# Optimization experiments

Hardware: AMD Instinct MI355X
Metric: run time of the kernel (lower is better)

Reference implementation:

```python
import jax, jax.numpy as jnp
import numpy as np

B = 16; DEMO = 5; COND = 50; QOI = 50
L = DEMO * (COND + 2 * QOI)  # 750
D = 1024; H = 16; HD = D // H; NL = 6; DFF = 4096
IN_DIM = 5; OUT_DIM = 2; MAXPOS = max(COND, QOI)
NEG = -1e9


def _build_consts():
    # token types per demo segment: 0=cond, 1=qoi_kv, 2=qoi_k (query)
    types, demo, pos = [], [], []
    for d in range(DEMO):
        types += [0] * COND + [1] * QOI + [2] * QOI
        demo += [d] * (COND + 2 * QOI)
        pos += list(range(COND)) + list(range(QOI)) + list(range(QOI))
    t = np.array(types); g = np.array(demo); p = np.array(pos)
    ti, tj = t[:, None], t[None, :]
    gi, gj = g[:, None], g[None, :]
    eye = np.arange(L)[:, None] == np.arange(L)[None, :]
    prev = (gj < gi) & (tj < 2)                      # attend to cond/qoi_kv of earlier demos
    same = (gj == gi) & ((tj == 0) | ((ti == 1) & (tj == 1)) | ((ti == 2) & eye))
    mask = prev | same                               # True = allowed
    out_idx = np.where(t == 2)[0]                    # qoi_k positions -> outputs
    return mask, p, out_idx


def setup_inputs():
    key = jax.random.key(0)
    ks = jax.random.split(key, 10)
    mask, pos, out_idx = _build_consts()
    s = 0.02
    return {
        'sequence': jax.random.normal(ks[0], (B, L, IN_DIM), jnp.float32),
        'pre_W': jax.random.normal(ks[1], (IN_DIM, D), jnp.float32) * s,
        'pre_b': jnp.zeros((D,), jnp.float32),
        'pe_table': jax.random.normal(ks[2], (MAXPOS, D), jnp.float32) * s,
        'Wqkv': jax.random.normal(ks[3], (NL, D, 3 * D), jnp.float32) * s,
        'bqkv': jnp.zeros((NL, 3 * D), jnp.float32),
        'Wo': jax.random.normal(ks[4], (NL, D, D), jnp.float32) * s,
        'bo': jnp.zeros((NL, D), jnp.float32),
        'ln1_g': jnp.ones((NL, D), jnp.float32), 'ln1_b': jnp.zeros((NL, D), jnp.float32),
        'ln2_g': jnp.ones((NL, D), jnp.float32), 'ln2_b': jnp.zeros((NL, D), jnp.float32),
        'W1': jax.random.normal(ks[5], (NL, D, DFF), jnp.float32) * s,
        'b1': jnp.zeros((NL, DFF), jnp.float32),
        'W2': jax.random.normal(ks[6], (NL, DFF, D), jnp.float32) * s,
        'b2': jnp.zeros((NL, D), jnp.float32),
        'post_W': jax.random.normal(ks[7], (D, OUT_DIM), jnp.float32) * s,
        'post_b': jnp.zeros((OUT_DIM,), jnp.float32),
        'basic_mask': jnp.asarray(mask),
        'index_pos': jnp.asarray(pos, jnp.int32),
        'out_idx': jnp.asarray(out_idx, jnp.int32),
    }


def _ln(x, g, b):
    m = jnp.mean(x, axis=-1, keepdims=True)
    v = jnp.var(x, axis=-1, keepdims=True)
    return (x - m) * jax.lax.rsqrt(v + 1e-5) * g + b


def _encoder(x, bias, Wqkv, bqkv, Wo, bo, ln1_g, ln1_b, ln2_g, ln2_b, W1, b1, W2, b2):
    scale = 1.0 / np.sqrt(HD)
    for l in range(NL):
        qkv = x @ Wqkv[l] + bqkv[l]                          # [B,L,3D]
        q, k, v = jnp.split(qkv, 3, axis=-1)
        hd = lambda t: t.reshape(B, L, H, HD).transpose(0, 2, 1, 3)
        q, k, v = hd(q), hd(k), hd(v)
        sc = jnp.einsum('bhqd,bhkd->bhqk', q, k) * scale + bias
        a = jax.nn.softmax(sc, axis=-1)
        o = jnp.einsum('bhqk,bhkd->bhqd', a, v).transpose(0, 2, 1, 3).reshape(B, L, D)
        x = _ln(x + o @ Wo[l] + bo[l], ln1_g[l], ln1_b[l])   # post-LN (torch default)
        h = jax.nn.gelu(x @ W1[l] + b1[l], approximate=False)
        x = _ln(x + h @ W2[l] + b2[l], ln2_g[l], ln2_b[l])
    return x


def reference(sequence, pre_W, pre_b, pe_table, Wqkv, bqkv, Wo, bo,
              ln1_g, ln1_b, ln2_g, ln2_b, W1, b1, W2, b2,
              post_W, post_b, basic_mask, index_pos, out_idx):
    x = sequence @ pre_W + pre_b + pe_table[index_pos]       # pre-projection + learned PE
    bias = jnp.where(basic_mask, 0.0, NEG)[None, None, :, :]  # ~basic_mask -> -inf additive
    x = _encoder(x, bias, Wqkv, bqkv, Wo, bo, ln1_g, ln1_b, ln2_g, ln2_b, W1, b1, W2, b2)
    y = x @ post_W + post_b                                  # [B,L,OUT_DIM]
    y = y[:, out_idx, :]                                     # select qoi_k outputs
    return y.reshape(B, DEMO, QOI, OUT_DIM)
```

## Files before the change

kernel.cpp:

```cpp
#include <hip/hip_runtime.h>


#define Bz  16
#define Lz  750
#define Dz  1024
#define Hz  16
#define HDz 64
#define NLz 6
#define DFFz 4096
#define Mz  (Bz*Lz)
#define VSTRIDE 768
#define QKVPART ((size_t)Bz*Hz*Lz*HDz)

typedef unsigned short u16;
typedef unsigned int   u32;
typedef unsigned long long u64;
typedef __attribute__((ext_vector_type(8))) short bf8;
typedef __attribute__((ext_vector_type(4))) float f4;
typedef __attribute__((ext_vector_type(4))) unsigned short u16x4;

__device__ __forceinline__ u16 f2b(float f){
  u32 u = __builtin_bit_cast(u32, f);
  u += 0x7fffu + ((u >> 16) & 1u);
  return (u16)(u >> 16);
}
__device__ __forceinline__ u32 cvtpk(float a, float b){
  u32 r;
  asm("v_cvt_pk_bf16_f32 %0, %1, %2" : "=v"(r) : "v"(a), "v"(b));
  return r;
}
__device__ __forceinline__ void glds16(const void* g, void* l){
  __builtin_amdgcn_global_load_lds((const __attribute__((address_space(1))) void*)g,
                                   (__attribute__((address_space(3))) void*)l, 16, 0, 0);
}

__global__ __launch_bounds__(256) void k_mask(u64* __restrict__ mb){
  const int idx = blockIdx.x*256 + threadIdx.x;
  if (idx >= Lz*12) return;
  const int q = idx / 12, kt = idx - q*12;
  const int gq = q/150, rq = q - gq*150;
  const int tq = rq < 50 ? 0 : (rq < 100 ? 1 : 2);
  u64 m = 0;
  for (int j = 0; j < 64; j++){
    const int k = kt*64 + j;
    if (k >= Lz) break;
    const int gk = k/150, rk = k - gk*150;
    const int tk = rk < 50 ? 0 : (rk < 100 ? 1 : 2);
    const bool prev = (gk < gq) && (tk < 2);
    const bool same = (gk == gq) && ((tk == 0) || (tq == 1 && tk == 1) || (tq == 2 && k == q));
    if (prev || same) m |= (1ull << j);
  }
  mb[idx] = m;
}

__global__ __launch_bounds__(256) void k_embed(const float* __restrict__ seq,
    const float* __restrict__ preW, const float* __restrict__ preb,
    const float* __restrict__ pe, float* __restrict__ x, u16* __restrict__ xb){
  const int m = blockIdx.x, t = threadIdx.x;
  const int l = m % Lz;
  const int r = l % 150;
  const int p = r < 50 ? r : (r < 100 ? r - 50 : r - 100);
  const float s0 = seq[m*5+0], s1 = seq[m*5+1], s2 = seq[m*5+2],
              s3 = seq[m*5+3], s4 = seq[m*5+4];
  const int d = t*4;
  f4 acc = *(const f4*)&preb[d];
  acc += *(const f4*)&pe[p*Dz + d];
  acc += s0 * *(const f4*)&preW[0*Dz + d];
  acc += s1 * *(const f4*)&preW[1*Dz + d];
  acc += s2 * *(const f4*)&preW[2*Dz + d];
  acc += s3 * *(const f4*)&preW[3*Dz + d];
  acc += s4 * *(const f4*)&preW[4*Dz + d];
  *(f4*)&x[(size_t)m*Dz + d] = acc;
  u16x4 hv = { f2b(acc.x), f2b(acc.y), f2b(acc.z), f2b(acc.w) };
  *(u16x4*)&xb[(size_t)m*Dz + d] = hv;
}

__global__ __launch_bounds__(256) void k_transpose(const float* __restrict__ W,
    u16* __restrict__ Wt, int K, int ldw){
  __shared__ float tile[32][33];
  const int tx = threadIdx.x, ty = threadIdx.y;
  const int n0 = blockIdx.x*32, k0 = blockIdx.y*32;
  #pragma unroll
  for (int i = 0; i < 4; i++){
    const int k = ty + i*8;
    tile[k][tx] = W[(size_t)(k0+k)*ldw + n0+tx];
  }
  __syncthreads();
  #pragma unroll
  for (int i = 0; i < 4; i++){
    const int n = ty + i*8;
    Wt[(size_t)(n0+n)*K + k0+tx] = f2b(tile[tx][n]);
  }
}

template<int EPI>
__global__ __launch_bounds__(256, 4) void k_gemm(
    const u16* __restrict__ A, const u16* __restrict__ Bt,
    int M, int N, int K, int lda, int ldc, int col0,
    const float* __restrict__ bias,
    float* __restrict__ xres, u16* __restrict__ outb, u16* __restrict__ vtb){
  __shared__ u16 As[128*64];
  __shared__ u16 Bs[128*64];
  const int t = threadIdx.x;
  const int m0 = blockIdx.x*128, n0 = blockIdx.y*128;
  const int w = t >> 6, lane = t & 63;
  const int wm = (w >> 1)*64, wn = (w & 1)*64;
  const int cl = lane & 15, g4 = lane >> 4;
  f4 acc[4][4] = {};
  const int srow = t >> 3, sg = t & 7;
  const int scol = (sg ^ (srow & 7)) * 8;
  const int lds_off = srow*64 + sg*8;
  for (int k0 = 0; k0 < K; k0 += 64){
    #pragma unroll
    for (int c = 0; c < 4; c++){
      int ra = m0 + c*32 + srow; ra = ra < M ? ra : M-1;
      glds16(A + (size_t)ra*lda + k0 + scol, &As[c*2048 + lds_off]);
      const int rb = n0 + c*32 + srow;
      glds16(Bt + (size_t)rb*K + k0 + scol, &Bs[c*2048 + lds_off]);
    }
    __syncthreads();
    #pragma unroll
    for (int kk = 0; kk < 2; kk++){
      const int ko = ((kk*4 + g4) ^ (cl & 7)) * 8;
      bf8 af[4], bfr[4];
      #pragma unroll
      for (int i = 0; i < 4; i++) af[i]  = *(const bf8*)&As[(wm + i*16 + cl)*64 + ko];
      #pragma unroll
      for (int j = 0; j < 4; j++) bfr[j] = *(const bf8*)&Bs[(wn + j*16 + cl)*64 + ko];
      #pragma unroll
      for (int i = 0; i < 4; i++)
        #pragma unroll
        for (int j = 0; j < 4; j++)
          acc[i][j] = __builtin_amdgcn_mfma_f32_16x16x32_bf16(af[i], bfr[j], acc[i][j], 0, 0, 0);
    }
    __syncthreads();
  }
  const int rl = g4*4;
  #pragma unroll
  for (int i = 0; i < 4; i++){
    #pragma unroll
    for (int j = 0; j < 4; j++){
      const int gn = n0 + wn + j*16 + cl;
      const float bsv = bias ? bias[gn] : 0.f;
      if constexpr (EPI == 0){
        const int part = gn >> 10;
        const int hh = (gn >> 6) & 15;
        const int dd = gn & 63;
        const int gm0 = m0 + wm + i*16 + rl;
        if (part == 2){
          if (gm0 + 3 < M){
            const int b = gm0 / Lz, lr0 = gm0 - b*Lz;
            const float v0 = acc[i][j][0] + bsv, v1 = acc[i][j][1] + bsv;
            const float v2 = acc[i][j][2] + bsv, v3 = acc[i][j][3] + bsv;
            if (lr0 <= Lz - 4){
              u32* dst = (u32*)&vtb[((size_t)(b*Hz + hh)*HDz + dd)*VSTRIDE + lr0];
              dst[0] = cvtpk(v0, v1);
              dst[1] = cvtpk(v2, v3);
            } else {
              #pragma unroll
              for (int r = 0; r < 4; r++){
                const int gm = gm0 + r;
                const int br = gm / Lz, lr = gm - br*Lz;
                vtb[((size_t)(br*Hz + hh)*HDz + dd)*VSTRIDE + lr] = f2b(acc[i][j][r] + bsv);
              }
            }
          }
        } else {
          #pragma unroll
          for (int r = 0; r < 4; r++){
            const int gm = gm0 + r;
            if (gm < M){
              const int b = gm / Lz, lr = gm - b*Lz;
              outb[(size_t)part*QKVPART + ((size_t)(b*Hz + hh)*Lz + lr)*HDz + dd]
                  = f2b(acc[i][j][r] + bsv);
            }
          }
        }
      } else {
        #pragma unroll
        for (int r = 0; r < 4; r++){
          const int gm = m0 + wm + i*16 + rl + r;
          if (gm < M){
            const float v = acc[i][j][r] + bsv;
            if constexpr (EPI == 1){
              xres[(size_t)gm*ldc + col0 + gn] += v;
            } else {
              const float ge = 0.5f*v*(1.0f + erff(v*0.70710678f));
              outb[(size_t)gm*ldc + col0 + gn] = f2b(ge);
            }
          }
        }
      }
    }
  }
}

__global__ __launch_bounds__(64, 4) void k_attn(const u16* __restrict__ qb,
    const u16* __restrict__ kb, const u16* __restrict__ vt,
    const u64* __restrict__ mb, u16* __restrict__ ob){
  __shared__ u32 Ps[1024];
  const int t = threadIdx.x;
  const int cl = t & 15, g4 = t >> 4;
  const int id = blockIdx.x;
  const int xcd = id & 7, j = id >> 3;
  const int bh = xcd*32 + (j/12);
  const int bx = j - (j/12)*12;
  const int b = bh >> 4, h = bh & 15;
  const u16* qhp = qb + (size_t)bh*(Lz*HDz);
  const u16* khp = kb + (size_t)bh*(Lz*HDz);
  const u16* vhp = vt + (size_t)bh*(HDz*VSTRIDE);
  const float SC = 0.18033688011112042f;
  const f4 z4 = {0.f, 0.f, 0.f, 0.f};

  for (int half = 0; half < 2; half++){
    const int c = half ? (23 - bx) : bx;
    const int q0 = c*32;
    bf8 qfr[2][2];
    int qc[2];
    #pragma unroll
    for (int qf = 0; qf < 2; qf++){
      const int q = q0 + qf*16 + cl;
      qc[qf] = q < Lz ? q : Lz-1;
      #pragma unroll
      for (int kk = 0; kk < 2; kk++)
        qfr[qf][kk] = *(const bf8*)&qhp[(size_t)qc[qf]*HDz + kk*32 + g4*8];
    }
    int qmax = q0 + 31; if (qmax > Lz-1) qmax = Lz-1;
    const int gqm = qmax/150;
    int kmax = gqm*150 + 100; if (qmax + 1 > kmax) kmax = qmax + 1;
    const int nt = (kmax + 63) >> 6;

    f4 oacc[4][2] = {};
    float mrun[2] = {-1e30f, -1e30f}, lrun[2] = {0.f, 0.f};

    for (int kt = 0; kt < nt; kt++){
      const int kstart = kt*64;
      u32 mlo[2], mhi[2];
      #pragma unroll
      for (int qf = 0; qf < 2; qf++){
        const u64 m = mb[qc[qf]*12 + kt];
        mlo[qf] = (u32)m; mhi[qf] = (u32)(m >> 32);
      }
      f4 sacc[4][2];
      __builtin_amdgcn_s_setprio(1);
      #pragma unroll
      for (int kk = 0; kk < 2; kk++){
        bf8 kfr[4];
        #pragma unroll
        for (int kf = 0; kf < 4; kf++)
          kfr[kf] = *(const bf8*)&khp[(size_t)(kstart + kf*16 + cl)*HDz + kk*32 + g4*8];
        #pragma unroll
        for (int kf = 0; kf < 4; kf++)
          #pragma unroll
          for (int qf = 0; qf < 2; qf++)
            sacc[kf][qf] = __builtin_amdgcn_mfma_f32_16x16x32_bf16(kfr[kf], qfr[qf][kk],
                             kk == 0 ? z4 : sacc[kf][qf], 0, 0, 0);
      }
      __builtin_amdgcn_s_setprio(0);
      float own0 = -1e30f, own1 = -1e30f;
      #pragma unroll
      for (int kf = 0; kf < 4; kf++){
        #pragma unroll
        for (int rr = 0; rr < 4; rr++){
          const float s0 = sacc[kf][0][rr]*SC;
          const float s1 = sacc[kf][1][rr]*SC;
          sacc[kf][0][rr] = s0; sacc[kf][1][rr] = s1;
          own0 = fmaxf(own0, s0); own1 = fmaxf(own1, s1);
        }
      }
      own0 = fmaxf(own0, __shfl_xor(own0, 16)); own0 = fmaxf(own0, __shfl_xor(own0, 32));
      own1 = fmaxf(own1, __shfl_xor(own1, 16)); own1 = fmaxf(own1, __shfl_xor(own1, 32));
      const float mn0 = fmaxf(mrun[0], own0), mn1 = fmaxf(mrun[1], own1);
      const float sc0 = exp2f(mrun[0] - mn0), sc1 = exp2f(mrun[1] - mn1);
      float sum0 = 0.f, sum1 = 0.f;
      #pragma unroll
      for (int kf = 0; kf < 4; kf++){
        #pragma unroll
        for (int qf = 0; qf < 2; qf++){
          const float mn = qf ? mn1 : mn0;
          const u32 w16 = ((kf & 2) ? mhi[qf] : mlo[qf]) >> ((kf & 1)*16);
          const u32 wq = w16 >> (g4*4);
          f4 p;
          #pragma unroll
          for (int rr = 0; rr < 4; rr++){
            const float pe = exp2f(sacc[kf][qf][rr] - mn);
            p[rr] = ((wq >> rr) & 1u) ? pe : 0.f;
            if (qf == 0) sum0 += p[rr]; else sum1 += p[rr];
          }
          const u32 lo = cvtpk(p[0], p[1]);
          const u32 hi = cvtpk(p[2], p[3]);
          const int kk = kf >> 1;
          const int tg4 = ((kf & 1) << 1) | (g4 >> 1);
          const int widx = (qf*2 + kk)*256 + tg4*64 + cl*4 + (g4 & 1)*2;
          *(u64*)&Ps[widx] = ((u64)hi << 32) | lo;
        }
      }
      sum0 += __shfl_xor(sum0, 16); sum0 += __shfl_xor(sum0, 32);
      sum1 += __shfl_xor(sum1, 16); sum1 += __shfl_xor(sum1, 32);
      lrun[0] = lrun[0]*sc0 + sum0; mrun[0] = mn0;
      lrun[1] = lrun[1]*sc1 + sum1; mrun[1] = mn1;
      #pragma unroll
      for (int df = 0; df < 4; df++){
        oacc[df][0] *= sc0;
        oacc[df][1] *= sc1;
      }
      __builtin_amdgcn_s_setprio(1);
      #pragma unroll
      for (int kk = 0; kk < 2; kk++){
        bf8 vfr[4];
        #pragma unroll
        for (int df = 0; df < 4; df++)
          vfr[df] = *(const bf8*)&vhp[(size_t)(df*16 + cl)*VSTRIDE + kstart + kk*32 + g4*8];
        bf8 pw[2];
        #pragma unroll
        for (int qf = 0; qf < 2; qf++)
          pw[qf] = *(const bf8*)&Ps[(qf*2 + kk)*256 + g4*64 + cl*4];
        #pragma unroll
        for (int df = 0; df < 4; df++)
          #pragma unroll
          for (int qf = 0; qf < 2; qf++)
            oacc[df][qf] = __builtin_amdgcn_mfma_f32_16x16x32_bf16(vfr[df], pw[qf], oacc[df][qf], 0, 0, 0);
      }
      __builtin_amdgcn_s_setprio(0);
    }
    #pragma unroll
    for (int qf = 0; qf < 2; qf++){
      const int q = q0 + qf*16 + cl;
      if (q < Lz){
        const float inv = 1.f / lrun[qf];
        #pragma unroll
        for (int df = 0; df < 4; df++){
          u16x4 hv = { f2b(oacc[df][qf][0]*inv), f2b(oacc[df][qf][1]*inv),
                       f2b(oacc[df][qf][2]*inv), f2b(oacc[df][qf][3]*inv) };
          *(u16x4*)&ob[((size_t)b*Lz + q)*Dz + h*HDz + df*16 + g4*4] = hv;
        }
      }
    }
  }
}

__global__ __launch_bounds__(256) void k_ln(float* __restrict__ x, u16* __restrict__ xb,
    const float* __restrict__ g, const float* __restrict__ bb){
  const int m = blockIdx.x, t = threadIdx.x;
  float* xr = x + (size_t)m*Dz;
  f4 v = *(const f4*)&xr[t*4];
  float s = v.x + v.y + v.z + v.w;
  float q = v.x*v.x + v.y*v.y + v.z*v.z + v.w*v.w;
  #pragma unroll
  for (int off = 1; off < 64; off <<= 1){
    s += __shfl_xor(s, off);
    q += __shfl_xor(q, off);
  }
  __shared__ float ss[4], sq[4];
  const int w = t >> 6;
  if ((t & 63) == 0){ ss[w] = s; sq[w] = q; }
  __syncthreads();
  s = ss[0] + ss[1] + ss[2] + ss[3];
  q = sq[0] + sq[1] + sq[2] + sq[3];
  const float mean = s * (1.f/1024.f);
  const float var  = q * (1.f/1024.f) - mean*mean;
  const float rs = rsqrtf(var + 1e-5f);
  const f4 gg = *(const f4*)&g[t*4];
  const f4 bv = *(const f4*)&bb[t*4];
  f4 o;
  o.x = (v.x - mean)*rs*gg.x + bv.x;
  o.y = (v.y - mean)*rs*gg.y + bv.y;
  o.z = (v.z - mean)*rs*gg.z + bv.z;
  o.w = (v.w - mean)*rs*gg.w + bv.w;
  *(f4*)&xr[t*4] = o;
  u16x4 hv = { f2b(o.x), f2b(o.y), f2b(o.z), f2b(o.w) };
  *(u16x4*)&xb[(size_t)m*Dz + t*4] = hv;
}

__global__ __launch_bounds__(64) void k_out(const float* __restrict__ x,
    const float* __restrict__ pw, const float* __restrict__ pb, float* __restrict__ out){
  const int bid = blockIdx.x, lane = threadIdx.x;
  const int b = bid / 250, oi = bid - b*250;
  const int dd = oi / 50, qq = oi - dd*50;
  const int l = dd*150 + 100 + qq;
  const float* xr = x + ((size_t)b*Lz + l)*Dz;
  float a0 = 0.f, a1 = 0.f;
  #pragma unroll
  for (int c = 0; c < 4; c++){
    const int d = c*256 + lane*4;
    const f4 v  = *(const f4*)&xr[d];
    const f4 p0 = *(const f4*)&pw[2*d];
    const f4 p1 = *(const f4*)&pw[2*d + 4];
    a0 += v.x*p0.x + v.y*p0.z + v.z*p1.x + v.w*p1.z;
    a1 += v.x*p0.y + v.y*p0.w + v.z*p1.y + v.w*p1.w;
  }
  #pragma unroll
  for (int off = 32; off > 0; off >>= 1){
    a0 += __shfl_xor(a0, off);
    a1 += __shfl_xor(a1, off);
  }
  if (lane == 0){
    out[(size_t)bid*2 + 0] = a0 + pb[0];
    out[(size_t)bid*2 + 1] = a1 + pb[1];
  }
}

extern "C" void kernel_launch(void* const* d_in, const int* in_sizes, int n_in,
                              void* d_out, int out_size, void* d_ws, size_t ws_size,
                              hipStream_t stream){
  (void)in_sizes; (void)n_in; (void)out_size; (void)ws_size;
  const float* seq   = (const float*)d_in[0];
  const float* preW  = (const float*)d_in[1];
  const float* preb  = (const float*)d_in[2];
  const float* pe    = (const float*)d_in[3];
  const float* Wqkv  = (const float*)d_in[4];
  const float* bqkv  = (const float*)d_in[5];
  const float* Wo    = (const float*)d_in[6];
  const float* bo    = (const float*)d_in[7];
  const float* ln1g  = (const float*)d_in[8];
  const float* ln1b  = (const float*)d_in[9];
  const float* ln2g  = (const float*)d_in[10];
  const float* ln2b  = (const float*)d_in[11];
  const float* W1    = (const float*)d_in[12];
  const float* b1    = (const float*)d_in[13];
  const float* W2    = (const float*)d_in[14];
  const float* b2    = (const float*)d_in[15];
  const float* postW = (const float*)d_in[16];
  const float* postb = (const float*)d_in[17];
  float* out = (float*)d_out;

  char* ws = (char*)d_ws;
  float* x  = (float*)(ws + 0);
  u16*   xb = (u16*)(ws + 49152000);
  u16*   R  = (u16*)(ws + 73728000);
  u16* qB = R;
  u16* kB = R + QKVPART;
  u16* oB = R + 2*QKVPART;
  u16* vT = (u16*)(ws + 147456000);
  u16* wt = (u16*)(ws + 172621824);
  u64* mbp = (u64*)(ws + 178913280);
  u16* hB = R;

  k_mask<<<36, 256, 0, stream>>>(mbp);
  k_embed<<<Mz, 256, 0, stream>>>(seq, preW, preb, pe, x, xb);
  const dim3 tb(32, 8);
  for (int l = 0; l < NLz; l++){
    k_transpose<<<dim3(96, 32), tb, 0, stream>>>(Wqkv + (size_t)l*1024*3072, wt, 1024, 3072);
    k_gemm<0><<<dim3(94, 24), 256, 0, stream>>>(xb, wt, Mz, 3072, 1024, 1024, 0, 0,
                                                bqkv + l*3072, nullptr, qB, vT);
    k_attn<<<3072, 64, 0, stream>>>(qB, kB, vT, mbp, oB);
    k_transpose<<<dim3(32, 32), tb, 0, stream>>>(Wo + (size_t)l*1024*1024, wt, 1024, 1024);
    k_gemm<1><<<dim3(94, 8), 256, 0, stream>>>(oB, wt, Mz, 1024, 1024, 1024, 1024, 0,
                                               bo + l*1024, x, nullptr, nullptr);
    k_ln<<<Mz, 256, 0, stream>>>(x, xb, ln1g + l*1024, ln1b + l*1024);
    for (int off = 0; off < 4096; off += 2048){
      k_transpose<<<dim3(64, 32), tb, 0, stream>>>(W1 + (size_t)l*1024*4096 + off, wt, 1024, 4096);
      k_gemm<2><<<dim3(94, 16), 256, 0, stream>>>(xb, wt, Mz, 2048, 1024, 1024, 4096, off,
                                                  b1 + l*4096 + off, nullptr, hB, nullptr);
    }
    for (int koff = 0; koff < 4096; koff += 2048){
      k_transpose<<<dim3(32, 64), tb, 0, stream>>>(W2 + (size_t)l*4096*1024 + (size_t)koff*1024,
                                                   wt, 2048, 1024);
      k_gemm<1><<<dim3(94, 8), 256, 0, stream>>>(hB + koff, wt, Mz, 1024, 2048, 4096, 1024, 0,
                                                 koff == 0 ? (b2 + l*1024) : nullptr, x, nullptr, nullptr);
    }
    k_ln<<<Mz, 256, 0, stream>>>(x, xb, ln2g + l*1024, ln2b + l*1024);
  }
  k_out<<<4000, 64, 0, stream>>>(x, postW, postb, out);
}
```

Measured before the change: 4.120 ms.

## Vectorize weight transpose with 64x64 tiles and split attention into one chunk per block

The weight transpose kernel now moves 64x64 tiles, reading float4 from global memory and writing 16 bf16 values per thread as two 16-byte stores, in place of scalar 32x32 tiles. This cuts instruction count and store transactions in the per-layer weight conversion. The attention kernel no longer pairs a short and a long query chunk in one block. It launches twice as many blocks with one 32-row chunk each, which raises parallelism but gives up the load balancing the pairing provided and loads Q and the mask setup more times overall.

```diff
diff --git a/kernel.cpp b/kernel.cpp
--- a/kernel.cpp
+++ b/kernel.cpp
@@ -16,6 +16,7 @@
 typedef unsigned int   u32;
 typedef unsigned long long u64;
 typedef __attribute__((ext_vector_type(8))) short bf8;
+typedef __attribute__((ext_vector_type(8))) unsigned short u16x8;
 typedef __attribute__((ext_vector_type(4))) float f4;
 typedef __attribute__((ext_vector_type(4))) unsigned short u16x4;
 
@@ -77,20 +78,26 @@
 
 __global__ __launch_bounds__(256) void k_transpose(const float* __restrict__ W,
     u16* __restrict__ Wt, int K, int ldw){
-  __shared__ float tile[32][33];
-  const int tx = threadIdx.x, ty = threadIdx.y;
-  const int n0 = blockIdx.x*32, k0 = blockIdx.y*32;
+  __shared__ float tile[64][69];
+  const int t = threadIdx.x;
+  const int n0 = blockIdx.x*64, k0 = blockIdx.y*64;
+  const int tx = t & 15, ty = t >> 4;
   #pragma unroll
   for (int i = 0; i < 4; i++){
-    const int k = ty + i*8;
-    tile[k][tx] = W[(size_t)(k0+k)*ldw + n0+tx];
+    const int k = ty + i*16;
+    *(f4*)&tile[k][tx*4] = *(const f4*)&W[(size_t)(k0+k)*ldw + n0 + tx*4];
   }
   __syncthreads();
-  #pragma unroll
-  for (int i = 0; i < 4; i++){
-    const int n = ty + i*8;
-    Wt[(size_t)(n0+n)*K + k0+tx] = f2b(tile[tx][n]);
-  }
+  const int nx = t >> 2, kq = t & 3;
+  u16 buf[16];
+  #pragma unroll
+  for (int e = 0; e < 16; e++)
+    buf[e] = f2b(tile[kq*16 + e][nx]);
+  u16x8 lo = { buf[0], buf[1], buf[2], buf[3], buf[4], buf[5], buf[6], buf[7] };
+  u16x8 hi = { buf[8], buf[9], buf[10], buf[11], buf[12], buf[13], buf[14], buf[15] };
+  u16* dst = &Wt[(size_t)(n0 + nx)*K + k0 + kq*16];
+  *(u16x8*)dst = lo;
+  *(u16x8*)(dst + 8) = hi;
 }
 
 template<int EPI>
@@ -203,8 +210,8 @@
   const int cl = t & 15, g4 = t >> 4;
   const int id = blockIdx.x;
   const int xcd = id & 7, j = id >> 3;
-  const int bh = xcd*32 + (j/12);
-  const int bx = j - (j/12)*12;
+  const int bh = xcd*32 + (j/24);
+  const int c = j - (j/24)*24;
   const int b = bh >> 4, h = bh & 15;
   const u16* qhp = qb + (size_t)bh*(Lz*HDz);
   const u16* khp = kb + (size_t)bh*(Lz*HDz);
@@ -212,128 +219,125 @@
   const float SC = 0.18033688011112042f;
   const f4 z4 = {0.f, 0.f, 0.f, 0.f};
 
-  for (int half = 0; half < 2; half++){
-    const int c = half ? (23 - bx) : bx;
-    const int q0 = c*32;
-    bf8 qfr[2][2];
-    int qc[2];
+  const int q0 = c*32;
+  bf8 qfr[2][2];
+  int qc[2];
+  #pragma unroll
+  for (int qf = 0; qf < 2; qf++){
+    const int q = q0 + qf*16 + cl;
+    qc[qf] = q < Lz ? q : Lz-1;
+    #pragma unroll
+    for (int kk = 0; kk < 2; kk++)
+      qfr[qf][kk] = *(const bf8*)&qhp[(size_t)qc[qf]*HDz + kk*32 + g4*8];
+  }
+  int qmax = q0 + 31; if (qmax > Lz-1) qmax = Lz-1;
+  const int gqm = qmax/150;
+  int kmax = gqm*150 + 100; if (qmax + 1 > kmax) kmax = qmax + 1;
+  const int nt = (kmax + 63) >> 6;
+
+  f4 oacc[4][2] = {};
+  float mrun[2] = {-1e30f, -1e30f}, lrun[2] = {0.f, 0.f};
+
+  for (int kt = 0; kt < nt; kt++){
+    const int kstart = kt*64;
+    u32 mlo[2], mhi[2];
     #pragma unroll
     for (int qf = 0; qf < 2; qf++){
-      const int q = q0 + qf*16 + cl;
-      qc[qf] = q < Lz ? q : Lz-1;
-      #pragma unroll
-      for (int kk = 0; kk < 2; kk++)
-        qfr[qf][kk] = *(const bf8*)&qhp[(size_t)qc[qf]*HDz + kk*32 + g4*8];
-    }
-    int qmax = q0 + 31; if (qmax > Lz-1) qmax = Lz-1;
-    const int gqm = qmax/150;
-    int kmax = gqm*150 + 100; if (qmax + 1 > kmax) kmax = qmax + 1;
-    const int nt = (kmax + 63) >> 6;
-
-    f4 oacc[4][2] = {};
-    float mrun[2] = {-1e30f, -1e30f}, lrun[2] = {0.f, 0.f};
-
-    for (int kt = 0; kt < nt; kt++){
-      const int kstart = kt*64;
-      u32 mlo[2], mhi[2];
+      const u64 m = mb[qc[qf]*12 + kt];
+      mlo[qf] = (u32)m; mhi[qf] = (u32)(m >> 32);
+    }
+    f4 sacc[4][2];
+    __builtin_amdgcn_s_setprio(1);
+    #pragma unroll
+    for (int kk = 0; kk < 2; kk++){
+      bf8 kfr[4];
+      #pragma unroll
+      for (int kf = 0; kf < 4; kf++)
+        kfr[kf] = *(const bf8*)&khp[(size_t)(kstart + kf*16 + cl)*HDz + kk*32 + g4*8];
+      #pragma unroll
+      for (int kf = 0; kf < 4; kf++)
+        #pragma unroll
+        for (int qf = 0; qf < 2; qf++)
+          sacc[kf][qf] = __builtin_amdgcn_mfma_f32_16x16x32_bf16(kfr[kf], qfr[qf][kk],
+                           kk == 0 ? z4 : sacc[kf][qf], 0, 0, 0);
+    }
+    __builtin_amdgcn_s_setprio(0);
+    float own0 = -1e30f, own1 = -1e30f;
+    #pragma unroll
+    for (int kf = 0; kf < 4; kf++){
+      #pragma unroll
+      for (int rr = 0; rr < 4; rr++){
+        const float s0 = sacc[kf][0][rr]*SC;
+        const float s1 = sacc[kf][1][rr]*SC;
+        sacc[kf][0][rr] = s0; sacc[kf][1][rr] = s1;
+        own0 = fmaxf(own0, s0); own1 = fmaxf(own1, s1);
+      }
+    }
+    own0 = fmaxf(own0, __shfl_xor(own0, 16)); own0 = fmaxf(own0, __shfl_xor(own0, 32));
+    own1 = fmaxf(own1, __shfl_xor(own1, 16)); own1 = fmaxf(own1, __shfl_xor(own1, 32));
+    const float mn0 = fmaxf(mrun[0], own0), mn1 = fmaxf(mrun[1], own1);
+    const float sc0 = exp2f(mrun[0] - mn0), sc1 = exp2f(mrun[1] - mn1);
+    float sum0 = 0.f, sum1 = 0.f;
+    #pragma unroll
+    for (int kf = 0; kf < 4; kf++){
       #pragma unroll
       for (int qf = 0; qf < 2; qf++){
-        const u64 m = mb[qc[qf]*12 + kt];
-        mlo[qf] = (u32)m; mhi[qf] = (u32)(m >> 32);
-      }
-      f4 sacc[4][2];
-      __builtin_amdgcn_s_setprio(1);
-      #pragma unroll
-      for (int kk = 0; kk < 2; kk++){
-        bf8 kfr[4];
-        #pragma unroll
-        for (int kf = 0; kf < 4; kf++)
-          kfr[kf] = *(const bf8*)&khp[(size_t)(kstart + kf*16 + cl)*HDz + kk*32 + g4*8];
-        #pragma unroll
-        for (int kf = 0; kf < 4; kf++)
-          #pragma unroll
-          for (int qf = 0; qf < 2; qf++)
-            sacc[kf][qf] = __builtin_amdgcn_mfma_f32_16x16x32_bf16(kfr[kf], qfr[qf][kk],
-                             kk == 0 ? z4 : sacc[kf][qf], 0, 0, 0);
-      }
-      __builtin_amdgcn_s_setprio(0);
-      float own0 = -1e30f, own1 = -1e30f;
-      #pragma unroll
-      for (int kf = 0; kf < 4; kf++){
+        const float mn = qf ? mn1 : mn0;
+        const u32 w16 = ((kf & 2) ? mhi[qf] : mlo[qf]) >> ((kf & 1)*16);
+        const u32 wq = w16 >> (g4*4);
+        f4 p;
         #pragma unroll
         for (int rr = 0; rr < 4; rr++){
-          const float s0 = sacc[kf][0][rr]*SC;
-          const float s1 = sacc[kf][1][rr]*SC;
-          sacc[kf][0][rr] = s0; sacc[kf][1][rr] = s1;
-          own0 = fmaxf(own0, s0); own1 = fmaxf(own1, s1);
+          const float pe = exp2f(sacc[kf][qf][rr] - mn);
+          p[rr] = ((wq >> rr) & 1u) ? pe : 0.f;
+          if (qf == 0) sum0 += p[rr]; else sum1 += p[rr];
         }
+        const u32 lo = cvtpk(p[0], p[1]);
+        const u32 hi = cvtpk(p[2], p[3]);
+        const int kk = kf >> 1;
+        const int tg4 = ((kf & 1) << 1) | (g4 >> 1);
+        const int widx = (qf*2 + kk)*256 + tg4*64 + cl*4 + (g4 & 1)*2;
+        *(u64*)&Ps[widx] = ((u64)hi << 32) | lo;
       }
-      own0 = fmaxf(own0, __shfl_xor(own0, 16)); own0 = fmaxf(own0, __shfl_xor(own0, 32));
-      own1 = fmaxf(own1, __shfl_xor(own1, 16)); own1 = fmaxf(own1, __shfl_xor(own1, 32));
-      const float mn0 = fmaxf(mrun[0], own0), mn1 = fmaxf(mrun[1], own1);
-      const float sc0 = exp2f(mrun[0] - mn0), sc1 = exp2f(mrun[1] - mn1);
-      float sum0 = 0.f, sum1 = 0.f;
-      #pragma unroll
-      for (int kf = 0; kf < 4; kf++){
-        #pragma unroll
-        for (int qf = 0; qf < 2; qf++){
-          const float mn = qf ? mn1 : mn0;
-          const u32 w16 = ((kf & 2) ? mhi[qf] : mlo[qf]) >> ((kf & 1)*16);
-          const u32 wq = w16 >> (g4*4);
-          f4 p;
-          #pragma unroll
-          for (int rr = 0; rr < 4; rr++){
-            const float pe = exp2f(sacc[kf][qf][rr] - mn);
-            p[rr] = ((wq >> rr) & 1u) ? pe : 0.f;
-            if (qf == 0) sum0 += p[rr]; else sum1 += p[rr];
-          }
-          const u32 lo = cvtpk(p[0], p[1]);
-          const u32 hi = cvtpk(p[2], p[3]);
-          const int kk = kf >> 1;
-          const int tg4 = ((kf & 1) << 1) | (g4 >> 1);
-          const int widx = (qf*2 + kk)*256 + tg4*64 + cl*4 + (g4 & 1)*2;
-          *(u64*)&Ps[widx] = ((u64)hi << 32) | lo;
-        }
-      }
-      sum0 += __shfl_xor(sum0, 16); sum0 += __shfl_xor(sum0, 32);
-      sum1 += __shfl_xor(sum1, 16); sum1 += __shfl_xor(sum1, 32);
-      lrun[0] = lrun[0]*sc0 + sum0; mrun[0] = mn0;
-      lrun[1] = lrun[1]*sc1 + sum1; mrun[1] = mn1;
-      #pragma unroll
-      for (int df = 0; df < 4; df++){
-        oacc[df][0] *= sc0;
-        oacc[df][1] *= sc1;
-      }
-      __builtin_amdgcn_s_setprio(1);
-      #pragma unroll
-      for (int kk = 0; kk < 2; kk++){
-        bf8 vfr[4];
-        #pragma unroll
-        for (int df = 0; df < 4; df++)
-          vfr[df] = *(const bf8*)&vhp[(size_t)(df*16 + cl)*VSTRIDE + kstart + kk*32 + g4*8];
-        bf8 pw[2];
+    }
+    sum0 += __shfl_xor(sum0, 16); sum0 += __shfl_xor(sum0, 32);
+    sum1 += __shfl_xor(sum1, 16); sum1 += __shfl_xor(sum1, 32);
+    lrun[0] = lrun[0]*sc0 + sum0; mrun[0] = mn0;
+    lrun[1] = lrun[1]*sc1 + sum1; mrun[1] = mn1;
+    #pragma unroll
+    for (int df = 0; df < 4; df++){
+      oacc[df][0] *= sc0;
+      oacc[df][1] *= sc1;
+    }
+    __builtin_amdgcn_s_setprio(1);
+    #pragma unroll
+    for (int kk = 0; kk < 2; kk++){
+      bf8 vfr[4];
+      #pragma unroll
+      for (int df = 0; df < 4; df++)
+        vfr[df] = *(const bf8*)&vhp[(size_t)(df*16 + cl)*VSTRIDE + kstart + kk*32 + g4*8];
+      bf8 pw[2];
+      #pragma unroll
+      for (int qf = 0; qf < 2; qf++)
+        pw[qf] = *(const bf8*)&Ps[(qf*2 + kk)*256 + g4*64 + cl*4];
+      #pragma unroll
+      for (int df = 0; df < 4; df++)
         #pragma unroll
         for (int qf = 0; qf < 2; qf++)
-          pw[qf] = *(const bf8*)&Ps[(qf*2 + kk)*256 + g4*64 + cl*4];
-        #pragma unroll
-        for (int df = 0; df < 4; df++)
-          #pragma unroll
-          for (int qf = 0; qf < 2; qf++)
-            oacc[df][qf] = __builtin_amdgcn_mfma_f32_16x16x32_bf16(vfr[df], pw[qf], oacc[df][qf], 0, 0, 0);
-      }
-      __builtin_amdgcn_s_setprio(0);
-    }
-    #pragma unroll
-    for (int qf = 0; qf < 2; qf++){
-      const int q = q0 + qf*16 + cl;
-      if (q < Lz){
-        const float inv = 1.f / lrun[qf];
-        #pragma unroll
-        for (int df = 0; df < 4; df++){
-          u16x4 hv = { f2b(oacc[df][qf][0]*inv), f2b(oacc[df][qf][1]*inv),
-                       f2b(oacc[df][qf][2]*inv), f2b(oacc[df][qf][3]*inv) };
-          *(u16x4*)&ob[((size_t)b*Lz + q)*Dz + h*HDz + df*16 + g4*4] = hv;
-        }
+          oacc[df][qf] = __builtin_amdgcn_mfma_f32_16x16x32_bf16(vfr[df], pw[qf], oacc[df][qf], 0, 0, 0);
+    }
+    __builtin_amdgcn_s_setprio(0);
+  }
+  #pragma unroll
+  for (int qf = 0; qf < 2; qf++){
+    const int q = q0 + qf*16 + cl;
+    if (q < Lz){
+      const float inv = 1.f / lrun[qf];
+      #pragma unroll
+      for (int df = 0; df < 4; df++){
+        u16x4 hv = { f2b(oacc[df][qf][0]*inv), f2b(oacc[df][qf][1]*inv),
+                     f2b(oacc[df][qf][2]*inv), f2b(oacc[df][qf][3]*inv) };
+        *(u16x4*)&ob[((size_t)b*Lz + q)*Dz + h*HDz + df*16 + g4*4] = hv;
       }
     }
   }
@@ -438,24 +442,23 @@
 
   k_mask<<<36, 256, 0, stream>>>(mbp);
   k_embed<<<Mz, 256, 0, stream>>>(seq, preW, preb, pe, x, xb);
-  const dim3 tb(32, 8);
   for (int l = 0; l < NLz; l++){
-    k_transpose<<<dim3(96, 32), tb, 0, stream>>>(Wqkv + (size_t)l*1024*3072, wt, 1024, 3072);
+    k_transpose<<<dim3(48, 16), 256, 0, stream>>>(Wqkv + (size_t)l*1024*3072, wt, 1024, 3072);
     k_gemm<0><<<dim3(94, 24), 256, 0, stream>>>(xb, wt, Mz, 3072, 1024, 1024, 0, 0,
                                                 bqkv + l*3072, nullptr, qB, vT);
-    k_attn<<<3072, 64, 0, stream>>>(qB, kB, vT, mbp, oB);
-    k_transpose<<<dim3(32, 32), tb, 0, stream>>>(Wo + (size_t)l*1024*1024, wt, 1024, 1024);
+    k_attn<<<6144, 64, 0, stream>>>(qB, kB, vT, mbp, oB);
+    k_transpose<<<dim3(16, 16), 256, 0, stream>>>(Wo + (size_t)l*1024*1024, wt, 1024, 1024);
     k_gemm<1><<<dim3(94, 8), 256, 0, stream>>>(oB, wt, Mz, 1024, 1024, 1024, 1024, 0,
                                                bo + l*1024, x, nullptr, nullptr);
     k_ln<<<Mz, 256, 0, stream>>>(x, xb, ln1g + l*1024, ln1b + l*1024);
     for (int off = 0; off < 4096; off += 2048){
-      k_transpose<<<dim3(64, 32), tb, 0, stream>>>(W1 + (size_t)l*1024*4096 + off, wt, 1024, 4096);
+      k_transpose<<<dim3(32, 16), 256, 0, stream>>>(W1 + (size_t)l*1024*4096 + off, wt, 1024, 4096);
       k_gemm<2><<<dim3(94, 16), 256, 0, stream>>>(xb, wt, Mz, 2048, 1024, 1024, 4096, off,
                                                   b1 + l*4096 + off, nullptr, hB, nullptr);
     }
     for (int koff = 0; koff < 4096; koff += 2048){
-      k_transpose<<<dim3(32, 64), tb, 0, stream>>>(W2 + (size_t)l*4096*1024 + (size_t)koff*1024,
-                                                   wt, 2048, 1024);
+      k_transpose<<<dim3(16, 32), 256, 0, stream>>>(W2 + (size_t)l*4096*1024 + (size_t)koff*1024,
+                                                    wt, 2048, 1024);
       k_gemm<1><<<dim3(94, 8), 256, 0, stream>>>(hB + koff, wt, Mz, 1024, 2048, 4096, 1024, 0,
                                                  koff == 0 ? (b2 + l*1024) : nullptr, x, nullptr, nullptr);
     }
```

After: 4.162 ms. About the same (+1.0%).
